# Optimization experiments

Measured on AMD Instinct MI355X. Metric: run time of the kernel, lower is better.

Reference implementation:

```python
import jax, jax.numpy as jnp
import numpy as np

N0, N1, F, H = 30000, 6000, 1024, 512
E00, E01, E10, E11 = 600000, 300000, 300000, 400000


def setup_inputs() -> dict:
    key = jax.random.key(0)
    keys = iter(jax.random.split(key, 64))

    def randn(shape, s=1.0):
        return jax.random.normal(next(keys), shape, dtype=jnp.float32) * s

    inp = {"feat0": randn((N0, F)), "feat1": randn((N1, F))}
    adj_specs = {"a00": (N0, N0, E00), "a01": (N0, N1, E01),
                 "a10": (N1, N0, E10), "a11a": (N1, N1, E11), "a11b": (N1, N1, E11)}
    for name, (ni, nj, e) in adj_specs.items():
        inp[name + "_row"] = jax.random.randint(next(keys), (e,), 0, ni, dtype=jnp.int32)
        inp[name + "_col"] = jax.random.randint(next(keys), (e,), 0, nj, dtype=jnp.int32)
        inp[name + "_val"] = jax.random.uniform(next(keys), (e,), dtype=jnp.float32)
    for rel in ["00", "01", "10", "11a", "11b"]:
        inp["W1_" + rel] = randn((F, H), 0.02)
        inp["W2_" + rel] = randn((H, H), 0.05)
        inp["W3_" + rel] = randn((H, H), 0.05)
    return inp


def _spmm(row, col, val, x, n_out):
    # sparse adjacency (n_out x n_in) @ x, COO edge-list form
    return jax.ops.segment_sum(val[:, None] * x[col], row, num_segments=n_out)


def reference(feat0, feat1,
              a00_row, a00_col, a00_val, a01_row, a01_col, a01_val,
              a10_row, a10_col, a10_val, a11a_row, a11a_col, a11a_val,
              a11b_row, a11b_col, a11b_val,
              W1_00, W1_01, W1_10, W1_11a, W1_11b,
              W2_00, W2_01, W2_10, W2_11a, W2_11b,
              W3_00, W3_01, W3_10, W3_11a, W3_11b):
    relu = jax.nn.relu

    def conv(row, col, val, x, W, n_out):
        # GraphConvolution(Sparse)Multi with identity act: adj @ (x @ W)
        return _spmm(row, col, val, x @ W, n_out)

    # Layer 1: relu(add_n over (i, j) edge types)
    e0_0 = relu(conv(a00_row, a00_col, a00_val, feat0, W1_00, N0)
                + conv(a01_row, a01_col, a01_val, feat1, W1_01, N0))
    e0_1 = relu(conv(a10_row, a10_col, a10_val, feat0, W1_10, N1)
                + conv(a11a_row, a11a_col, a11a_val, feat1, W1_11a, N1)
                + conv(a11b_row, a11b_col, a11b_val, feat1, W1_11b, N1))

    # Layer 2: original does embeddings1 = embeddings0 + embeddings1 (python list
    # concat), so embeddings1[j] == embeddings0[j] -> layer-2 inputs are e0.
    e2_0 = relu(conv(a00_row, a00_col, a00_val, e0_0, W2_00, N0)
                + conv(a01_row, a01_col, a01_val, e0_1, W2_01, N0))
    e2_1 = relu(conv(a10_row, a10_col, a10_val, e0_0, W2_10, N1)
                + conv(a11a_row, a11a_col, a11a_val, e0_1, W2_11a, N1)
                + conv(a11b_row, a11b_col, a11b_val, e0_1, W2_11b, N1))

    # Layer 3: inputs are layer-2 outputs (same list-concat quirk); no relu.
    e3_0 = (conv(a00_row, a00_col, a00_val, e2_0, W3_00, N0)
            + conv(a01_row, a01_col, a01_val, e2_1, W3_01, N0))
    e3_1 = (conv(a10_row, a10_col, a10_val, e2_0, W3_10, N1)
            + conv(a11a_row, a11a_col, a11a_val, e2_1, W3_11a, N1)
            + conv(a11b_row, a11b_col, a11b_val, e2_1, W3_11b, N1))

    # Final: concat([e0, embeddings1(=e0), e3]) per object type; stack obj types
    # along node axis for a single output array.
    out0 = jnp.concatenate([e0_0, e0_0, e3_0], axis=1)  # [N0, 3H]
    out1 = jnp.concatenate([e0_1, e0_1, e3_1], axis=1)  # [N1, 3H]
    return jnp.concatenate([out0, out1], axis=0)  # [N0+N1, 3H]
```

## Files before the change

kernel.cpp:

```cpp
#include <hip/hip_runtime.h>
#include <stdint.h>

#define N0 30000
#define N1 6000
#define FDIM 1024
#define HDIM 512
#define E00 600000
#define E01 300000
#define E10 300000
#define E11A 400000
#define E11B 400000
#define NE_TOT (E00 + E01 + E10 + E11A + E11B)

typedef __attribute__((ext_vector_type(4))) float f32x4;
typedef __attribute__((ext_vector_type(8))) __bf16 bf16x8;

__device__ __forceinline__ unsigned short f2bf(float f) {
  unsigned u = __float_as_uint(f);
  u += 0x7fffu + ((u >> 16) & 1u);
  return (unsigned short)(u >> 16);
}

__device__ __forceinline__ void gload16(const void* g, void* l) {
  __builtin_amdgcn_global_load_lds((const __attribute__((address_space(1))) void*)g,
                                   (__attribute__((address_space(3))) void*)l, 16, 0, 0);
}

__global__ void conv_bf16_kernel(const float* __restrict__ src, unsigned short* __restrict__ dst, int n4) {
  int gid = blockIdx.x * blockDim.x + threadIdx.x;
  if (gid >= n4) return;
  float4 v = ((const float4*)src)[gid];
  ushort4 o;
  o.x = f2bf(v.x); o.y = f2bf(v.y); o.z = f2bf(v.z); o.w = f2bf(v.w);
  ((ushort4*)dst)[gid] = o;
}

__global__ void conv_weights_kernel(const float* __restrict__ w00, const float* __restrict__ w10,
                                    const float* __restrict__ w01, const float* __restrict__ w11a,
                                    const float* __restrict__ w11b,
                                    unsigned short* __restrict__ dst0, unsigned short* __restrict__ dst1, int K) {
  int gid = blockIdx.x * blockDim.x + threadIdx.x;
  int total0 = 1024 * K;
  int total1 = 1536 * K;
  if (gid < total0) {
    int n = gid / K, k = gid - n * K;
    const float* w = (n < 512) ? w00 : w10;
    int nn = n & 511;
    dst0[gid] = f2bf(w[(size_t)k * 512 + nn]);
  } else if (gid < total0 + total1) {
    int g = gid - total0;
    int n = g / K, k = g - n * K;
    const float* w = (n < 512) ? w01 : ((n < 1024) ? w11a : w11b);
    int nn = n & 511;
    dst1[g] = f2bf(w[(size_t)k * 512 + nn]);
  }
}

__global__ void conv_wk_kernel(const float* __restrict__ w00, const float* __restrict__ w01,
                               const float* __restrict__ w10, const float* __restrict__ w11a,
                               const float* __restrict__ w11b,
                               unsigned short* __restrict__ dst0, unsigned short* __restrict__ dst1) {
  int gid = blockIdx.x * blockDim.x + threadIdx.x;
  const int T0 = 512 * 1024;
  const int T1 = 512 * 1536;
  if (gid < T0) {
    int n = gid >> 10, k = gid & 1023;
    const float* w = (k < 512) ? w00 : w01;
    dst0[gid] = f2bf(w[(size_t)(k & 511) * 512 + n]);
  } else if (gid < T0 + T1) {
    int g = gid - T0;
    int n = g / 1536, k = g - n * 1536;
    const float* w = (k < 512) ? w10 : ((k < 1024) ? w11a : w11b);
    dst1[g] = f2bf(w[(size_t)(k & 511) * 512 + n]);
  }
}

__global__ void zero_ints(int* p, int n) {
  int g = blockIdx.x * blockDim.x + threadIdx.x;
  if (g < n) p[g] = 0;
}

__global__ void hist5(const int* __restrict__ r0, const int* __restrict__ r1, const int* __restrict__ r2,
                      const int* __restrict__ r3, const int* __restrict__ r4,
                      int* c0, int* c1, int* c2, int* c3, int* c4) {
  int g = blockIdx.x * blockDim.x + threadIdx.x;
  const int* r; int* c; int e;
  if (g < E00) { r = r0; c = c0; e = g; }
  else if (g < E00 + E01) { r = r1; c = c1; e = g - E00; }
  else if (g < E00 + E01 + E10) { r = r2; c = c2; e = g - (E00 + E01); }
  else if (g < E00 + E01 + E10 + E11A) { r = r3; c = c3; e = g - (E00 + E01 + E10); }
  else if (g < NE_TOT) { r = r4; c = c4; e = g - (E00 + E01 + E10 + E11A); }
  else return;
  atomicAdd(&c[r[e]], 1);
}

__global__ __launch_bounds__(1024) void scan5p(int* c0, int* rp0, int* c1, int* rp1,
                                               int* c2, int* rp2, int* c3, int* rp3,
                                               int* c4, int* rp4) {
  int b = blockIdx.x;
  int* cnt; int* rp; int n;
  if (b == 0) { cnt = c0; rp = rp0; n = N0; }
  else if (b == 1) { cnt = c1; rp = rp1; n = N0; }
  else if (b == 2) { cnt = c2; rp = rp2; n = N1; }
  else if (b == 3) { cnt = c3; rp = rp3; n = N1; }
  else { cnt = c4; rp = rp4; n = N1; }
  __shared__ int wsum[16];
  const int tid = threadIdx.x, lane = tid & 63, w = tid >> 6;
  int carry = 0;
  for (int base = 0; base < n; base += 1024) {
    int i = base + tid;
    int v = (i < n) ? cnt[i] : 0;
    int x = v;
    #pragma unroll
    for (int d = 1; d < 64; d <<= 1) {
      int y = __shfl_up(x, d, 64);
      if (lane >= d) x += y;
    }
    if (lane == 63) wsum[w] = x;
    __syncthreads();
    if (w == 0) {
      int t = (lane < 16) ? wsum[lane] : 0;
      #pragma unroll
      for (int d = 1; d < 16; d <<= 1) {
        int y = __shfl_up(t, d, 64);
        if (lane >= d) t += y;
      }
      if (lane < 16) wsum[lane] = t;
    }
    __syncthreads();
    int wpref = (w > 0) ? wsum[w - 1] : 0;
    int excl = carry + wpref + (x - v);
    if (i < n) { rp[i] = excl; cnt[i] = excl; }
    carry += wsum[15];
    __syncthreads();
  }
  if (tid == 0) rp[n] = carry;
}

__global__ void scatter5(const int* __restrict__ r0, const int* __restrict__ q0, const float* __restrict__ v0,
                         int* cur0, int* sc0, float* sv0,
                         const int* __restrict__ r1, const int* __restrict__ q1, const float* __restrict__ v1,
                         int* cur1, int* sc1, float* sv1,
                         const int* __restrict__ r2, const int* __restrict__ q2, const float* __restrict__ v2,
                         int* cur2, int* sc2, float* sv2,
                         const int* __restrict__ r3, const int* __restrict__ q3, const float* __restrict__ v3,
                         int* cur3, int* sc3, float* sv3,
                         const int* __restrict__ r4, const int* __restrict__ q4, const float* __restrict__ v4,
                         int* cur4, int* sc4, float* sv4) {
  int g = blockIdx.x * blockDim.x + threadIdx.x;
  const int* r; const int* q; const float* v; int* cur; int* sc; float* sv; int e;
  if (g < E00) { r = r0; q = q0; v = v0; cur = cur0; sc = sc0; sv = sv0; e = g; }
  else if (g < E00 + E01) { r = r1; q = q1; v = v1; cur = cur1; sc = sc1; sv = sv1; e = g - E00; }
  else if (g < E00 + E01 + E10) { r = r2; q = q2; v = v2; cur = cur2; sc = sc2; sv = sv2; e = g - (E00 + E01); }
  else if (g < E00 + E01 + E10 + E11A) { r = r3; q = q3; v = v3; cur = cur3; sc = sc3; sv = sv3; e = g - (E00 + E01 + E10); }
  else if (g < NE_TOT) { r = r4; q = q4; v = v4; cur = cur4; sc = sc4; sv = sv4; e = g - (E00 + E01 + E10 + E11A); }
  else return;
  int row = r[e];
  int p = atomicAdd(&cur[row], 1);
  sc[p] = q[e];
  sv[p] = v[e];
}

#define BM 128
#define BN 128
#define BK 64

template<int MODE>
__global__ __launch_bounds__(256) void gemm_bf16(const unsigned short* __restrict__ A,
                                                 const unsigned short* __restrict__ Bt,
                                                 void* __restrict__ Cv,
                                                 int M, int N, int K, int nbx, int ldc) {
  __shared__ unsigned short As[BM * BK];
  __shared__ unsigned short Bs[BN * BK];
  const int nwg = gridDim.x;
  const int orig = blockIdx.x;
  const int q = nwg >> 3, rr = nwg & 7;
  const int xcd = orig & 7, pos = orig >> 3;
  const int wg = (xcd < rr ? xcd * (q + 1) : rr * (q + 1) + (xcd - rr) * q) + pos;
  const int bx = wg % nbx;
  const int by = wg / nbx;

  const int tid = threadIdx.x;
  const int lane = tid & 63;
  const int wid = tid >> 6;
  const int m0 = bx * BM;
  const int n0 = by * BN;
  const int wm = (wid >> 1) * 64;
  const int wn = (wid & 1) * 64;

  f32x4 acc[4][4] = {};

  const int srow = wid * 32 + (lane >> 3);
  const int scol = (lane & 7) * 8;

  for (int k0 = 0; k0 < K; k0 += BK) {
    #pragma unroll
    for (int c = 0; c < 4; ++c) {
      int gr = m0 + srow + c * 8;
      if (gr > M - 1) gr = M - 1;
      gload16(A + (size_t)gr * K + k0 + scol, As + (wid * 32 + c * 8) * BK);
      int gn = n0 + srow + c * 8;
      gload16(Bt + (size_t)gn * K + k0 + scol, Bs + (wid * 32 + c * 8) * BK);
    }
    __syncthreads();
    #pragma unroll
    for (int ks = 0; ks < 2; ++ks) {
      bf16x8 af[4], bfr[4];
      #pragma unroll
      for (int i = 0; i < 4; i++)
        af[i] = *(const bf16x8*)(As + (wm + i * 16 + (lane & 15)) * BK + ks * 32 + (lane >> 4) * 8);
      #pragma unroll
      for (int j = 0; j < 4; j++)
        bfr[j] = *(const bf16x8*)(Bs + (wn + j * 16 + (lane & 15)) * BK + ks * 32 + (lane >> 4) * 8);
      #pragma unroll
      for (int i = 0; i < 4; i++)
        #pragma unroll
        for (int j = 0; j < 4; j++)
          acc[i][j] = __builtin_amdgcn_mfma_f32_16x16x32_bf16(af[i], bfr[j], acc[i][j], 0, 0, 0);
    }
    __syncthreads();
  }

  #pragma unroll
  for (int i = 0; i < 4; i++) {
    int rbase = m0 + wm + i * 16 + (lane >> 4) * 4;
    #pragma unroll
    for (int j = 0; j < 4; j++) {
      int col = n0 + wn + j * 16 + (lane & 15);
      #pragma unroll
      for (int r = 0; r < 4; r++) {
        int row = rbase + r;
        if (row < M) {
          float v = acc[i][j][r];
          if (MODE == 1) v = fmaxf(v, 0.f);
          if (MODE == 2) ((float*)Cv)[(size_t)row * ldc + col] = v;
          else ((unsigned short*)Cv)[(size_t)row * ldc + col] = f2bf(v);
        }
      }
    }
  }
}

__device__ __forceinline__ void acc8(float* acc, float v, const uint4& u) {
  acc[0] += v * __uint_as_float(u.x << 16);
  acc[1] += v * __uint_as_float(u.x & 0xffff0000u);
  acc[2] += v * __uint_as_float(u.y << 16);
  acc[3] += v * __uint_as_float(u.y & 0xffff0000u);
  acc[4] += v * __uint_as_float(u.z << 16);
  acc[5] += v * __uint_as_float(u.z & 0xffff0000u);
  acc[6] += v * __uint_as_float(u.w << 16);
  acc[7] += v * __uint_as_float(u.w & 0xffff0000u);
}

__device__ __forceinline__ void gather_row(const int* __restrict__ ci, const float* __restrict__ cv,
                                           const unsigned short* __restrict__ gb, int ld,
                                           int e, int e1, float* acc) {
  for (; e + 7 < e1; e += 8) {
    int c0 = ci[e], c1 = ci[e + 1], c2 = ci[e + 2], c3 = ci[e + 3];
    int c4 = ci[e + 4], c5 = ci[e + 5], c6 = ci[e + 6], c7 = ci[e + 7];
    float v0 = cv[e], v1 = cv[e + 1], v2 = cv[e + 2], v3 = cv[e + 3];
    float v4 = cv[e + 4], v5 = cv[e + 5], v6 = cv[e + 6], v7 = cv[e + 7];
    uint4 u0 = *(const uint4*)(gb + (size_t)c0 * ld);
    uint4 u1 = *(const uint4*)(gb + (size_t)c1 * ld);
    uint4 u2 = *(const uint4*)(gb + (size_t)c2 * ld);
    uint4 u3 = *(const uint4*)(gb + (size_t)c3 * ld);
    uint4 u4 = *(const uint4*)(gb + (size_t)c4 * ld);
    uint4 u5 = *(const uint4*)(gb + (size_t)c5 * ld);
    uint4 u6 = *(const uint4*)(gb + (size_t)c6 * ld);
    uint4 u7 = *(const uint4*)(gb + (size_t)c7 * ld);
    acc8(acc, v0, u0); acc8(acc, v1, u1); acc8(acc, v2, u2); acc8(acc, v3, u3);
    acc8(acc, v4, u4); acc8(acc, v5, u5); acc8(acc, v6, u6); acc8(acc, v7, u7);
  }
  for (; e < e1; ++e) {
    int c = ci[e];
    float v = cv[e];
    uint4 u = *(const uint4*)(gb + (size_t)c * ld);
    acc8(acc, v, u);
  }
}

__global__ __launch_bounds__(256) void spmm_kernel(
    int nrows, int nseg,
    const int* __restrict__ rp0, const int* __restrict__ ci0, const float* __restrict__ cv0,
    const unsigned short* __restrict__ g0, int ld0, int off0,
    const int* __restrict__ rp1, const int* __restrict__ ci1, const float* __restrict__ cv1,
    const unsigned short* __restrict__ g1, int ld1, int off1,
    const int* __restrict__ rp2, const int* __restrict__ ci2, const float* __restrict__ cv2,
    const unsigned short* __restrict__ g2, int ld2, int off2,
    unsigned short* __restrict__ ebf,
    float* __restrict__ outp, int out_row0) {
  const int lane = threadIdx.x & 63;
  const int r = blockIdx.x * 4 + (threadIdx.x >> 6);
  if (r >= nrows) return;
  float acc[8] = {0.f, 0.f, 0.f, 0.f, 0.f, 0.f, 0.f, 0.f};
  for (int s = 0; s < nseg; ++s) {
    const int* rp; const int* ci; const float* cv; const unsigned short* g; int ld, off;
    if (s == 0) { rp = rp0; ci = ci0; cv = cv0; g = g0; ld = ld0; off = off0; }
    else if (s == 1) { rp = rp1; ci = ci1; cv = cv1; g = g1; ld = ld1; off = off1; }
    else { rp = rp2; ci = ci2; cv = cv2; g = g2; ld = ld2; off = off2; }
    int e = __builtin_amdgcn_readfirstlane(rp[r]);
    int e1 = __builtin_amdgcn_readfirstlane(rp[r + 1]);
    gather_row(ci, cv, g + off + lane * 8, ld, e, e1, acc);
  }
  #pragma unroll
  for (int i = 0; i < 8; i++) acc[i] = fmaxf(acc[i], 0.f);
  uint4 o;
  o.x = (unsigned)f2bf(acc[0]) | ((unsigned)f2bf(acc[1]) << 16);
  o.y = (unsigned)f2bf(acc[2]) | ((unsigned)f2bf(acc[3]) << 16);
  o.z = (unsigned)f2bf(acc[4]) | ((unsigned)f2bf(acc[5]) << 16);
  o.w = (unsigned)f2bf(acc[6]) | ((unsigned)f2bf(acc[7]) << 16);
  *(uint4*)(ebf + (size_t)r * HDIM + lane * 8) = o;
  float4 v0; v0.x = acc[0]; v0.y = acc[1]; v0.z = acc[2]; v0.w = acc[3];
  float4 v1; v1.x = acc[4]; v1.y = acc[5]; v1.z = acc[6]; v1.w = acc[7];
  size_t base = (size_t)(out_row0 + r) * 1536 + lane * 8;
  *(float4*)(outp + base) = v0;
  *(float4*)(outp + base + 4) = v1;
  *(float4*)(outp + base + 512) = v0;
  *(float4*)(outp + base + 516) = v1;
}

__global__ __launch_bounds__(256) void spmm_sep(
    int nrows, int nseg,
    const int* __restrict__ rp0, const int* __restrict__ ci0, const float* __restrict__ cv0,
    const unsigned short* __restrict__ t0,
    const int* __restrict__ rp1, const int* __restrict__ ci1, const float* __restrict__ cv1,
    const unsigned short* __restrict__ t1,
    const int* __restrict__ rp2, const int* __restrict__ ci2, const float* __restrict__ cv2,
    const unsigned short* __restrict__ t2,
    unsigned short* __restrict__ outp, int ld_out) {
  const int lane = threadIdx.x & 63;
  const int r = blockIdx.x * 4 + (threadIdx.x >> 6);
  if (r >= nrows) return;
  for (int s = 0; s < nseg; ++s) {
    const int* rp; const int* ci; const float* cv; const unsigned short* t;
    if (s == 0) { rp = rp0; ci = ci0; cv = cv0; t = t0; }
    else if (s == 1) { rp = rp1; ci = ci1; cv = cv1; t = t1; }
    else { rp = rp2; ci = ci2; cv = cv2; t = t2; }
    float acc[8] = {0.f, 0.f, 0.f, 0.f, 0.f, 0.f, 0.f, 0.f};
    int e = __builtin_amdgcn_readfirstlane(rp[r]);
    int e1 = __builtin_amdgcn_readfirstlane(rp[r + 1]);
    gather_row(ci, cv, t + lane * 8, HDIM, e, e1, acc);
    uint4 o;
    o.x = (unsigned)f2bf(acc[0]) | ((unsigned)f2bf(acc[1]) << 16);
    o.y = (unsigned)f2bf(acc[2]) | ((unsigned)f2bf(acc[3]) << 16);
    o.z = (unsigned)f2bf(acc[4]) | ((unsigned)f2bf(acc[5]) << 16);
    o.w = (unsigned)f2bf(acc[6]) | ((unsigned)f2bf(acc[7]) << 16);
    *(uint4*)(outp + (size_t)r * ld_out + s * HDIM + lane * 8) = o;
  }
}

extern "C" void kernel_launch(void* const* d_in, const int* in_sizes, int n_in,
                              void* d_out, int out_size, void* d_ws, size_t ws_size,
                              hipStream_t stream) {
  const float* feat0 = (const float*)d_in[0];
  const float* feat1 = (const float*)d_in[1];
  const int* a00_row = (const int*)d_in[2];
  const int* a00_col = (const int*)d_in[3];
  const float* a00_val = (const float*)d_in[4];
  const int* a01_row = (const int*)d_in[5];
  const int* a01_col = (const int*)d_in[6];
  const float* a01_val = (const float*)d_in[7];
  const int* a10_row = (const int*)d_in[8];
  const int* a10_col = (const int*)d_in[9];
  const float* a10_val = (const float*)d_in[10];
  const int* a11a_row = (const int*)d_in[11];
  const int* a11a_col = (const int*)d_in[12];
  const float* a11a_val = (const float*)d_in[13];
  const int* a11b_row = (const int*)d_in[14];
  const int* a11b_col = (const int*)d_in[15];
  const float* a11b_val = (const float*)d_in[16];

  const float *W1[5], *W2[5], *W3[5];
  if (in_sizes[18] == 512 * 512) {
    for (int r = 0; r < 5; r++) {
      W1[r] = (const float*)d_in[17 + 3 * r];
      W2[r] = (const float*)d_in[18 + 3 * r];
      W3[r] = (const float*)d_in[19 + 3 * r];
    }
  } else {
    for (int r = 0; r < 5; r++) {
      W1[r] = (const float*)d_in[17 + r];
      W2[r] = (const float*)d_in[22 + r];
      W3[r] = (const float*)d_in[27 + r];
    }
  }

  char* ws = (char*)d_ws;
  size_t off = 0;
  auto alloc = [&](size_t bytes) -> char* {
    char* p = ws + off;
    off += (bytes + 255) & ~(size_t)255;
    return p;
  };
  unsigned short* feat0b = (unsigned short*)alloc((size_t)N0 * FDIM * 2);
  unsigned short* feat1b = (unsigned short*)alloc((size_t)N1 * FDIM * 2);
  unsigned short* Wt1_0 = (unsigned short*)alloc((size_t)1024 * 1024 * 2);
  unsigned short* Wt1_1 = (unsigned short*)alloc((size_t)1536 * 1024 * 2);
  unsigned short* Wt2_0 = (unsigned short*)alloc((size_t)512 * 1024 * 2);
  unsigned short* Wt2_1 = (unsigned short*)alloc((size_t)512 * 1536 * 2);
  unsigned short* Wt3_0 = (unsigned short*)alloc((size_t)512 * 1024 * 2);
  unsigned short* Wt3_1 = (unsigned short*)alloc((size_t)512 * 1536 * 2);
  unsigned short* G0 = (unsigned short*)alloc((size_t)N0 * 1024 * 2);
  unsigned short* G1 = (unsigned short*)alloc((size_t)N1 * 1536 * 2);
  unsigned short* e0_0 = (unsigned short*)alloc((size_t)N0 * HDIM * 2);
  unsigned short* e0_1 = (unsigned short*)alloc((size_t)N1 * HDIM * 2);
  int* cur = (int*)alloc((size_t)(2 * N0 + 3 * N1) * 4);
  int* cur00 = cur;
  int* cur01 = cur + N0;
  int* cur10 = cur + 2 * N0;
  int* cur11a = cur + 2 * N0 + N1;
  int* cur11b = cur + 2 * N0 + 2 * N1;
  int* rp00 = (int*)alloc((N0 + 1) * 4);
  int* rp01 = (int*)alloc((N0 + 1) * 4);
  int* rp10 = (int*)alloc((N1 + 1) * 4);
  int* rp11a = (int*)alloc((N1 + 1) * 4);
  int* rp11b = (int*)alloc((N1 + 1) * 4);
  int* sc00 = (int*)alloc((size_t)E00 * 4);
  float* sv00 = (float*)alloc((size_t)E00 * 4);
  int* sc01 = (int*)alloc((size_t)E01 * 4);
  float* sv01 = (float*)alloc((size_t)E01 * 4);
  int* sc10 = (int*)alloc((size_t)E10 * 4);
  float* sv10 = (float*)alloc((size_t)E10 * 4);
  int* sc11a = (int*)alloc((size_t)E11A * 4);
  float* sv11a = (float*)alloc((size_t)E11A * 4);
  int* sc11b = (int*)alloc((size_t)E11B * 4);
  float* sv11b = (float*)alloc((size_t)E11B * 4);
  unsigned short* e2_0 = feat0b;
  unsigned short* e2_1 = feat1b;
  float* out = (float*)d_out;

  conv_bf16_kernel<<<(N0 * FDIM / 4 + 255) / 256, 256, 0, stream>>>(feat0, feat0b, N0 * FDIM / 4);
  conv_bf16_kernel<<<(N1 * FDIM / 4 + 255) / 256, 256, 0, stream>>>(feat1, feat1b, N1 * FDIM / 4);
  conv_weights_kernel<<<(2560 * 1024 + 255) / 256, 256, 0, stream>>>(W1[0], W1[2], W1[1], W1[3], W1[4], Wt1_0, Wt1_1, 1024);
  conv_wk_kernel<<<(512 * 2560 + 255) / 256, 256, 0, stream>>>(W2[0], W2[1], W2[2], W2[3], W2[4], Wt2_0, Wt2_1);
  conv_wk_kernel<<<(512 * 2560 + 255) / 256, 256, 0, stream>>>(W3[0], W3[1], W3[2], W3[3], W3[4], Wt3_0, Wt3_1);

  int ncur = 2 * N0 + 3 * N1;
  zero_ints<<<(ncur + 255) / 256, 256, 0, stream>>>(cur, ncur);
  hist5<<<(NE_TOT + 255) / 256, 256, 0, stream>>>(a00_row, a01_row, a10_row, a11a_row, a11b_row,
                                                  cur00, cur01, cur10, cur11a, cur11b);
  scan5p<<<5, 1024, 0, stream>>>(cur00, rp00, cur01, rp01, cur10, rp10, cur11a, rp11a, cur11b, rp11b);
  scatter5<<<(NE_TOT + 255) / 256, 256, 0, stream>>>(
      a00_row, a00_col, a00_val, cur00, sc00, sv00,
      a01_row, a01_col, a01_val, cur01, sc01, sv01,
      a10_row, a10_col, a10_val, cur10, sc10, sv10,
      a11a_row, a11a_col, a11a_val, cur11a, sc11a, sv11a,
      a11b_row, a11b_col, a11b_val, cur11b, sc11b, sv11b);

  dim3 blk(256);
  int nbx0 = (N0 + BM - 1) / BM;
  int nbx1 = (N1 + BM - 1) / BM;

  gemm_bf16<0><<<dim3(nbx0 * 8), blk, 0, stream>>>(feat0b, Wt1_0, G0, N0, 1024, 1024, nbx0, 1024);
  gemm_bf16<0><<<dim3(nbx1 * 12), blk, 0, stream>>>(feat1b, Wt1_1, G1, N1, 1536, 1024, nbx1, 1536);
  spmm_kernel<<<(N0 + 3) / 4, blk, 0, stream>>>(N0, 2,
      rp00, sc00, sv00, G0, 1024, 0,
      rp01, sc01, sv01, G1, 1536, 0,
      nullptr, nullptr, nullptr, nullptr, 0, 0,
      e0_0, out, 0);
  spmm_kernel<<<(N1 + 3) / 4, blk, 0, stream>>>(N1, 3,
      rp10, sc10, sv10, G0, 1024, 512,
      rp11a, sc11a, sv11a, G1, 1536, 512,
      rp11b, sc11b, sv11b, G1, 1536, 1024,
      e0_1, out, N0);

  spmm_sep<<<(N0 + 3) / 4, blk, 0, stream>>>(N0, 2,
      rp00, sc00, sv00, e0_0,
      rp01, sc01, sv01, e0_1,
      nullptr, nullptr, nullptr, nullptr,
      G0, 1024);
  spmm_sep<<<(N1 + 3) / 4, blk, 0, stream>>>(N1, 3,
      rp10, sc10, sv10, e0_0,
      rp11a, sc11a, sv11a, e0_1,
      rp11b, sc11b, sv11b, e0_1,
      G1, 1536);
  gemm_bf16<1><<<dim3(nbx0 * 4), blk, 0, stream>>>(G0, Wt2_0, e2_0, N0, 512, 1024, nbx0, 512);
  gemm_bf16<1><<<dim3(nbx1 * 4), blk, 0, stream>>>(G1, Wt2_1, e2_1, N1, 512, 1536, nbx1, 512);

  spmm_sep<<<(N0 + 3) / 4, blk, 0, stream>>>(N0, 2,
      rp00, sc00, sv00, e2_0,
      rp01, sc01, sv01, e2_1,
      nullptr, nullptr, nullptr, nullptr,
      G0, 1024);
  spmm_sep<<<(N1 + 3) / 4, blk, 0, stream>>>(N1, 3,
      rp10, sc10, sv10, e2_0,
      rp11a, sc11a, sv11a, e2_1,
      rp11b, sc11b, sv11b, e2_1,
      G1, 1536);
  gemm_bf16<2><<<dim3(nbx0 * 4), blk, 0, stream>>>(G0, Wt3_0, out + 1024, N0, 512, 1024, nbx0, 1536);
  gemm_bf16<2><<<dim3(nbx1 * 4), blk, 0, stream>>>(G1, Wt3_1, out + (size_t)N0 * 1536 + 1024, N1, 512, 1536, nbx1, 1536);
}
```

Measured before the change: 1.376 ms.

## Merge paired per-type GEMM and SpMM launches into single grouped kernels

Each pair of GEMM launches (node type 0 and 1) becomes one gemm_pair launch that dispatches on block index. The SpMM pairs become grid-stride persistent kernels with a fixed 2048-block grid covering both node types. Final fp32 outputs now use nontemporal stores. The intent is to cut launch gaps and tail underutilisation from the small N1 kernels running alone, at the cost of extra branching and a fixed grid size that may not balance well.

After: 1.352 ms. Within noise of the previous version (-1.7%).

```diff
diff --git a/kernel.cpp b/kernel.cpp
--- a/kernel.cpp
+++ b/kernel.cpp
@@ -165,20 +165,23 @@
 #define BN 128
 #define BK 64
 
+struct GemmArgs {
+  const unsigned short* A;
+  const unsigned short* Bt;
+  void* C;
+  int M, N, K, nbx, ldc, nwg;
+};
+
 template<int MODE>
-__global__ __launch_bounds__(256) void gemm_bf16(const unsigned short* __restrict__ A,
-                                                 const unsigned short* __restrict__ Bt,
-                                                 void* __restrict__ Cv,
-                                                 int M, int N, int K, int nbx, int ldc) {
+__device__ __forceinline__ void gemm_body(const GemmArgs& g, int orig) {
   __shared__ unsigned short As[BM * BK];
   __shared__ unsigned short Bs[BN * BK];
-  const int nwg = gridDim.x;
-  const int orig = blockIdx.x;
+  const int nwg = g.nwg;
   const int q = nwg >> 3, rr = nwg & 7;
   const int xcd = orig & 7, pos = orig >> 3;
   const int wg = (xcd < rr ? xcd * (q + 1) : rr * (q + 1) + (xcd - rr) * q) + pos;
-  const int bx = wg % nbx;
-  const int by = wg / nbx;
+  const int bx = wg % g.nbx;
+  const int by = wg / g.nbx;
 
   const int tid = threadIdx.x;
   const int lane = tid & 63;
@@ -187,6 +190,7 @@
   const int n0 = by * BN;
   const int wm = (wid >> 1) * 64;
   const int wn = (wid & 1) * 64;
+  const int M = g.M, K = g.K;
 
   f32x4 acc[4][4] = {};
 
@@ -198,9 +202,9 @@
     for (int c = 0; c < 4; ++c) {
       int gr = m0 + srow + c * 8;
       if (gr > M - 1) gr = M - 1;
-      gload16(A + (size_t)gr * K + k0 + scol, As + (wid * 32 + c * 8) * BK);
+      gload16(g.A + (size_t)gr * K + k0 + scol, As + (wid * 32 + c * 8) * BK);
       int gn = n0 + srow + c * 8;
-      gload16(Bt + (size_t)gn * K + k0 + scol, Bs + (wid * 32 + c * 8) * BK);
+      gload16(g.Bt + (size_t)gn * K + k0 + scol, Bs + (wid * 32 + c * 8) * BK);
     }
     __syncthreads();
     #pragma unroll
@@ -233,12 +237,20 @@
         if (row < M) {
           float v = acc[i][j][r];
           if (MODE == 1) v = fmaxf(v, 0.f);
-          if (MODE == 2) ((float*)Cv)[(size_t)row * ldc + col] = v;
-          else ((unsigned short*)Cv)[(size_t)row * ldc + col] = f2bf(v);
+          if (MODE == 2)
+            __builtin_nontemporal_store(v, &((float*)g.C)[(size_t)row * g.ldc + col]);
+          else
+            ((unsigned short*)g.C)[(size_t)row * g.ldc + col] = f2bf(v);
         }
       }
     }
   }
+}
+
+template<int MODE>
+__global__ __launch_bounds__(256) void gemm_pair(GemmArgs ga, GemmArgs gb) {
+  if ((int)blockIdx.x < ga.nwg) gemm_body<MODE>(ga, blockIdx.x);
+  else gemm_body<MODE>(gb, blockIdx.x - ga.nwg);
 }
 
 __device__ __forceinline__ void acc8(float* acc, float v, const uint4& u) {
@@ -279,73 +291,97 @@
   }
 }
 
-__global__ __launch_bounds__(256) void spmm_kernel(
-    int nrows, int nseg,
-    const int* __restrict__ rp0, const int* __restrict__ ci0, const float* __restrict__ cv0,
-    const unsigned short* __restrict__ g0, int ld0, int off0,
-    const int* __restrict__ rp1, const int* __restrict__ ci1, const float* __restrict__ cv1,
-    const unsigned short* __restrict__ g1, int ld1, int off1,
-    const int* __restrict__ rp2, const int* __restrict__ ci2, const float* __restrict__ cv2,
-    const unsigned short* __restrict__ g2, int ld2, int off2,
-    unsigned short* __restrict__ ebf,
-    float* __restrict__ outp, int out_row0) {
+struct Seg {
+  const int* rp; const int* ci; const float* cv;
+  const unsigned short* tbl; int ld; int off;
+};
+
+__device__ __forceinline__ void gather_seg(const Seg& s, int r, int lane, float* acc) {
+  int e = __builtin_amdgcn_readfirstlane(s.rp[r]);
+  int e1 = __builtin_amdgcn_readfirstlane(s.rp[r + 1]);
+  gather_row(s.ci, s.cv, s.tbl + s.off + lane * 8, s.ld, e, e1, acc);
+}
+
+struct Spmm1Set {
+  int nrows, nseg;
+  Seg s0, s1, s2;
+  unsigned short* ebf;
+  float* outp;
+};
+
+__global__ __launch_bounds__(256) void spmm1_pair(Spmm1Set A, Spmm1Set B) {
   const int lane = threadIdx.x & 63;
-  const int r = blockIdx.x * 4 + (threadIdx.x >> 6);
-  if (r >= nrows) return;
-  float acc[8] = {0.f, 0.f, 0.f, 0.f, 0.f, 0.f, 0.f, 0.f};
-  for (int s = 0; s < nseg; ++s) {
-    const int* rp; const int* ci; const float* cv; const unsigned short* g; int ld, off;
-    if (s == 0) { rp = rp0; ci = ci0; cv = cv0; g = g0; ld = ld0; off = off0; }
-    else if (s == 1) { rp = rp1; ci = ci1; cv = cv1; g = g1; ld = ld1; off = off1; }
-    else { rp = rp2; ci = ci2; cv = cv2; g = g2; ld = ld2; off = off2; }
-    int e = __builtin_amdgcn_readfirstlane(rp[r]);
-    int e1 = __builtin_amdgcn_readfirstlane(rp[r + 1]);
-    gather_row(ci, cv, g + off + lane * 8, ld, e, e1, acc);
-  }
-  #pragma unroll
-  for (int i = 0; i < 8; i++) acc[i] = fmaxf(acc[i], 0.f);
-  uint4 o;
-  o.x = (unsigned)f2bf(acc[0]) | ((unsigned)f2bf(acc[1]) << 16);
-  o.y = (unsigned)f2bf(acc[2]) | ((unsigned)f2bf(acc[3]) << 16);
-  o.z = (unsigned)f2bf(acc[4]) | ((unsigned)f2bf(acc[5]) << 16);
-  o.w = (unsigned)f2bf(acc[6]) | ((unsigned)f2bf(acc[7]) << 16);
-  *(uint4*)(ebf + (size_t)r * HDIM + lane * 8) = o;
-  float4 v0; v0.x = acc[0]; v0.y = acc[1]; v0.z = acc[2]; v0.w = acc[3];
-  float4 v1; v1.x = acc[4]; v1.y = acc[5]; v1.z = acc[6]; v1.w = acc[7];
-  size_t base = (size_t)(out_row0 + r) * 1536 + lane * 8;
-  *(float4*)(outp + base) = v0;
-  *(float4*)(outp + base + 4) = v1;
-  *(float4*)(outp + base + 512) = v0;
-  *(float4*)(outp + base + 516) = v1;
-}
-
-__global__ __launch_bounds__(256) void spmm_sep(
-    int nrows, int nseg,
-    const int* __restrict__ rp0, const int* __restrict__ ci0, const float* __restrict__ cv0,
-    const unsigned short* __restrict__ t0,
-    const int* __restrict__ rp1, const int* __restrict__ ci1, const float* __restrict__ cv1,
-    const unsigned short* __restrict__ t1,
-    const int* __restrict__ rp2, const int* __restrict__ ci2, const float* __restrict__ cv2,
-    const unsigned short* __restrict__ t2,
-    unsigned short* __restrict__ outp, int ld_out) {
-  const int lane = threadIdx.x & 63;
-  const int r = blockIdx.x * 4 + (threadIdx.x >> 6);
-  if (r >= nrows) return;
-  for (int s = 0; s < nseg; ++s) {
-    const int* rp; const int* ci; const float* cv; const unsigned short* t;
-    if (s == 0) { rp = rp0; ci = ci0; cv = cv0; t = t0; }
-    else if (s == 1) { rp = rp1; ci = ci1; cv = cv1; t = t1; }
-    else { rp = rp2; ci = ci2; cv = cv2; t = t2; }
+  const int gw = blockIdx.x * 4 + (threadIdx.x >> 6);
+  const int W = gridDim.x * 4;
+  const int total = A.nrows + B.nrows;
+  for (int r0 = gw; r0 < total; r0 += W) {
+    bool useA = (r0 < A.nrows);
+    int r = useA ? r0 : r0 - A.nrows;
     float acc[8] = {0.f, 0.f, 0.f, 0.f, 0.f, 0.f, 0.f, 0.f};
-    int e = __builtin_amdgcn_readfirstlane(rp[r]);
-    int e1 = __builtin_amdgcn_readfirstlane(rp[r + 1]);
-    gather_row(ci, cv, t + lane * 8, HDIM, e, e1, acc);
+    {
+      Seg s = useA ? A.s0 : B.s0;
+      gather_seg(s, r, lane, acc);
+    }
+    {
+      Seg s = useA ? A.s1 : B.s1;
+      gather_seg(s, r, lane, acc);
+    }
+    if (!useA) {
+      gather_seg(B.s2, r, lane, acc);
+    }
+    #pragma unroll
+    for (int i = 0; i < 8; i++) acc[i] = fmaxf(acc[i], 0.f);
+    unsigned short* ebf = useA ? A.ebf : B.ebf;
+    float* outp = useA ? A.outp : B.outp;
     uint4 o;
     o.x = (unsigned)f2bf(acc[0]) | ((unsigned)f2bf(acc[1]) << 16);
     o.y = (unsigned)f2bf(acc[2]) | ((unsigned)f2bf(acc[3]) << 16);
     o.z = (unsigned)f2bf(acc[4]) | ((unsigned)f2bf(acc[5]) << 16);
     o.w = (unsigned)f2bf(acc[6]) | ((unsigned)f2bf(acc[7]) << 16);
-    *(uint4*)(outp + (size_t)r * ld_out + s * HDIM + lane * 8) = o;
+    *(uint4*)(ebf + (size_t)r * HDIM + lane * 8) = o;
+    f32x4 v0 = {acc[0], acc[1], acc[2], acc[3]};
+    f32x4 v1 = {acc[4], acc[5], acc[6], acc[7]};
+    size_t base = (size_t)r * 1536 + lane * 8;
+    __builtin_nontemporal_store(v0, (f32x4*)(outp + base));
+    __builtin_nontemporal_store(v1, (f32x4*)(outp + base + 4));
+    __builtin_nontemporal_store(v0, (f32x4*)(outp + base + 512));
+    __builtin_nontemporal_store(v1, (f32x4*)(outp + base + 516));
+  }
+}
+
+struct SepSet {
+  int nrows, nseg;
+  Seg s0, s1, s2;
+  unsigned short* outp;
+  int ldo;
+};
+
+__global__ __launch_bounds__(256) void spmm_sep_pair(SepSet A, SepSet B) {
+  const int lane = threadIdx.x & 63;
+  const int gw = blockIdx.x * 4 + (threadIdx.x >> 6);
+  const int W = gridDim.x * 4;
+  const int total = A.nrows + B.nrows;
+  for (int r0 = gw; r0 < total; r0 += W) {
+    bool useA = (r0 < A.nrows);
+    int r = useA ? r0 : r0 - A.nrows;
+    unsigned short* outp = useA ? A.outp : B.outp;
+    int ldo = useA ? A.ldo : B.ldo;
+    int nseg = useA ? A.nseg : B.nseg;
+    #pragma unroll
+    for (int sidx = 0; sidx < 3; ++sidx) {
+      if (sidx >= nseg) break;
+      Seg s = (sidx == 0) ? (useA ? A.s0 : B.s0)
+            : (sidx == 1) ? (useA ? A.s1 : B.s1)
+                          : (useA ? A.s2 : B.s2);
+      float acc[8] = {0.f, 0.f, 0.f, 0.f, 0.f, 0.f, 0.f, 0.f};
+      gather_seg(s, r, lane, acc);
+      uint4 o;
+      o.x = (unsigned)f2bf(acc[0]) | ((unsigned)f2bf(acc[1]) << 16);
+      o.y = (unsigned)f2bf(acc[2]) | ((unsigned)f2bf(acc[3]) << 16);
+      o.z = (unsigned)f2bf(acc[4]) | ((unsigned)f2bf(acc[5]) << 16);
+      o.w = (unsigned)f2bf(acc[6]) | ((unsigned)f2bf(acc[7]) << 16);
+      *(uint4*)(outp + (size_t)r * ldo + sidx * HDIM + lane * 8) = o;
+    }
   }
 }
 
@@ -450,43 +486,54 @@
   dim3 blk(256);
   int nbx0 = (N0 + BM - 1) / BM;
   int nbx1 = (N1 + BM - 1) / BM;
-
-  gemm_bf16<0><<<dim3(nbx0 * 8), blk, 0, stream>>>(feat0b, Wt1_0, G0, N0, 1024, 1024, nbx0, 1024);
-  gemm_bf16<0><<<dim3(nbx1 * 12), blk, 0, stream>>>(feat1b, Wt1_1, G1, N1, 1536, 1024, nbx1, 1536);
-  spmm_kernel<<<(N0 + 3) / 4, blk, 0, stream>>>(N0, 2,
-      rp00, sc00, sv00, G0, 1024, 0,
-      rp01, sc01, sv01, G1, 1536, 0,
-      nullptr, nullptr, nullptr, nullptr, 0, 0,
-      e0_0, out, 0);
-  spmm_kernel<<<(N1 + 3) / 4, blk, 0, stream>>>(N1, 3,
-      rp10, sc10, sv10, G0, 1024, 512,
-      rp11a, sc11a, sv11a, G1, 1536, 512,
-      rp11b, sc11b, sv11b, G1, 1536, 1024,
-      e0_1, out, N0);
-
-  spmm_sep<<<(N0 + 3) / 4, blk, 0, stream>>>(N0, 2,
-      rp00, sc00, sv00, e0_0,
-      rp01, sc01, sv01, e0_1,
-      nullptr, nullptr, nullptr, nullptr,
-      G0, 1024);
-  spmm_sep<<<(N1 + 3) / 4, blk, 0, stream>>>(N1, 3,
-      rp10, sc10, sv10, e0_0,
-      rp11a, sc11a, sv11a, e0_1,
-      rp11b, sc11b, sv11b, e0_1,
-      G1, 1536);
-  gemm_bf16<1><<<dim3(nbx0 * 4), blk, 0, stream>>>(G0, Wt2_0, e2_0, N0, 512, 1024, nbx0, 512);
-  gemm_bf16<1><<<dim3(nbx1 * 4), blk, 0, stream>>>(G1, Wt2_1, e2_1, N1, 512, 1536, nbx1, 512);
-
-  spmm_sep<<<(N0 + 3) / 4, blk, 0, stream>>>(N0, 2,
-      rp00, sc00, sv00, e2_0,
-      rp01, sc01, sv01, e2_1,
-      nullptr, nullptr, nullptr, nullptr,
-      G0, 1024);
-  spmm_sep<<<(N1 + 3) / 4, blk, 0, stream>>>(N1, 3,
-      rp10, sc10, sv10, e2_0,
-      rp11a, sc11a, sv11a, e2_1,
-      rp11b, sc11b, sv11b, e2_1,
-      G1, 1536);
-  gemm_bf16<2><<<dim3(nbx0 * 4), blk, 0, stream>>>(G0, Wt3_0, out + 1024, N0, 512, 1024, nbx0, 1536);
-  gemm_bf16<2><<<dim3(nbx1 * 4), blk, 0, stream>>>(G1, Wt3_1, out + (size_t)N0 * 1536 + 1024, N1, 512, 1536, nbx1, 1536);
-}
+  const int SPMM_GRID = 2048;
+
+  Seg sg00_G = {rp00, sc00, sv00, G0, 1024, 0};
+  Seg sg01_G = {rp01, sc01, sv01, G1, 1536, 0};
+  Seg sg10_G = {rp10, sc10, sv10, G0, 1024, 512};
+  Seg sg11a_G = {rp11a, sc11a, sv11a, G1, 1536, 512};
+  Seg sg11b_G = {rp11b, sc11b, sv11b, G1, 1536, 1024};
+
+  {
+    GemmArgs ga = {feat0b, Wt1_0, G0, N0, 1024, 1024, nbx0, 1024, nbx0 * 8};
+    GemmArgs gb = {feat1b, Wt1_1, G1, N1, 1536, 1024, nbx1, 1536, nbx1 * 12};
+    gemm_pair<0><<<dim3(ga.nwg + gb.nwg), blk, 0, stream>>>(ga, gb);
+  }
+  {
+    Spmm1Set A = {N0, 2, sg00_G, sg01_G, Seg{}, e0_0, out};
+    Spmm1Set B = {N1, 3, sg10_G, sg11a_G, sg11b_G, e0_1, out + (size_t)N0 * 1536};
+    spmm1_pair<<<dim3(SPMM_GRID), blk, 0, stream>>>(A, B);
+  }
+
+  {
+    Seg a0 = {rp00, sc00, sv00, e0_0, HDIM, 0};
+    Seg a1 = {rp01, sc01, sv01, e0_1, HDIM, 0};
+    Seg b0 = {rp10, sc10, sv10, e0_0, HDIM, 0};
+    Seg b1 = {rp11a, sc11a, sv11a, e0_1, HDIM, 0};
+    Seg b2 = {rp11b, sc11b, sv11b, e0_1, HDIM, 0};
+    SepSet A = {N0, 2, a0, a1, Seg{}, G0, 1024};
+    SepSet B = {N1, 3, b0, b1, b2, G1, 1536};
+    spmm_sep_pair<<<dim3(SPMM_GRID), blk, 0, stream>>>(A, B);
+  }
+  {
+    GemmArgs ga = {G0, Wt2_0, e2_0, N0, 512, 1024, nbx0, 512, nbx0 * 4};
+    GemmArgs gb = {G1, Wt2_1, e2_1, N1, 512, 1536, nbx1, 512, nbx1 * 4};
+    gemm_pair<1><<<dim3(ga.nwg + gb.nwg), blk, 0, stream>>>(ga, gb);
+  }
+
+  {
+    Seg a0 = {rp00, sc00, sv00, e2_0, HDIM, 0};
+    Seg a1 = {rp01, sc01, sv01, e2_1, HDIM, 0};
+    Seg b0 = {rp10, sc10, sv10, e2_0, HDIM, 0};
+    Seg b1 = {rp11a, sc11a, sv11a, e2_1, HDIM, 0};
+    Seg b2 = {rp11b, sc11b, sv11b, e2_1, HDIM, 0};
+    SepSet A = {N0, 2, a0, a1, Seg{}, G0, 1024};
+    SepSet B = {N1, 3, b0, b1, b2, G1, 1536};
+    spmm_sep_pair<<<dim3(SPMM_GRID), blk, 0, stream>>>(A, B);
+  }
+  {
+    GemmArgs ga = {G0, Wt3_0, out + 1024, N0, 512, 1024, nbx0, 1536, nbx0 * 4};
+    GemmArgs gb = {G1, Wt3_1, out + (size_t)N0 * 1536 + 1024, N1, 512, 1536, nbx1, 1536, nbx1 * 4};
+    gemm_pair<2><<<dim3(ga.nwg + gb.nwg), blk, 0, stream>>>(ga, gb);
+  }
+}
```
